# Kernel optimization log

Hardware: AMD Instinct MI355X
Metric: run time of the kernel (lower is better)

Reference implementation:

```python
import jax, jax.numpy as jnp
import numpy as np

N_NODES = 50000
N_EDGES = 800000
IN_C, HID, OUT_C = 128, 128, 16
N_GRAPHS = 128


def setup_inputs() -> dict:
    key = jax.random.key(0)
    ks = jax.random.split(key, 8)
    x = jax.random.normal(ks[0], (N_NODES, IN_C), dtype=jnp.float32)
    edge_index = jax.random.randint(ks[1], (2, N_EDGES), 0, N_NODES, dtype=jnp.int64)
    batch = jnp.sort(jax.random.randint(ks[2], (N_NODES,), 0, N_GRAPHS, dtype=jnp.int64))
    s1 = 1.0 / np.sqrt(IN_C)
    s2 = 1.0 / np.sqrt(HID)
    W1 = jax.random.normal(ks[3], (IN_C, HID), dtype=jnp.float32) * s1
    b1 = jnp.zeros((HID,), dtype=jnp.float32)
    W2 = jax.random.normal(ks[4], (HID, HID), dtype=jnp.float32) * s2
    b2 = jnp.zeros((HID,), dtype=jnp.float32)
    Wfc = jax.random.normal(ks[5], (HID, OUT_C), dtype=jnp.float32) * s2
    bfc = jnp.zeros((OUT_C,), dtype=jnp.float32)
    return {"x": x, "edge_index": edge_index, "batch": batch,
            "W1": W1, "b1": b1, "W2": W2, "b2": b2, "Wfc": Wfc, "bfc": bfc}


def _gcn_conv(x, W, b, src, dst, deg_inv_sqrt, n_nodes):
    # linear transform first (PyG order), then normalized sparse aggregation
    h = x @ W  # [N, H]
    norm = deg_inv_sqrt[src] * deg_inv_sqrt[dst]  # [E+N] (self-loops appended)
    msgs = h[src] * norm[:, None]  # [E+N, H] dominant gather
    agg = jax.ops.segment_sum(msgs, dst, num_segments=n_nodes)
    return agg + b


def reference(x, edge_index, batch, W1, b1, W2, b2, Wfc, bfc):
    n = x.shape[0]
    loops = jnp.arange(n, dtype=edge_index.dtype)
    src = jnp.concatenate([edge_index[0], loops])
    dst = jnp.concatenate([edge_index[1], loops])
    # symmetric normalization with self-loops: deg computed on dst
    deg = jax.ops.segment_sum(jnp.ones_like(src, dtype=x.dtype), dst, num_segments=n)
    deg_inv_sqrt = jnp.where(deg > 0, jax.lax.rsqrt(jnp.maximum(deg, 1.0)), 0.0)

    h = jax.nn.relu(_gcn_conv(x, W1, b1, src, dst, deg_inv_sqrt, n))
    h = jax.nn.relu(_gcn_conv(h, W2, b2, src, dst, deg_inv_sqrt, n))

    # global mean pool over graph ids
    sums = jax.ops.segment_sum(h, batch, num_segments=N_GRAPHS)
    counts = jax.ops.segment_sum(jnp.ones((n,), dtype=h.dtype), batch, num_segments=N_GRAPHS)
    pooled = sums / jnp.maximum(counts, 1.0)[:, None]  # [G, H]

    logits = pooled @ Wfc + bfc  # [G, OUT_C]
    return jax.nn.log_softmax(logits, axis=1)
```

## Files before the change

kernel.cpp:

```cpp
#include <hip/hip_runtime.h>

#define N_NODES  50000
#define N_EDGES  800000
#define HID      128
#define OUT_C    16
#define N_GRAPHS 128
#define MAXDEG   64
#define NSLICE   6250
#define EPB      8192

typedef __attribute__((ext_vector_type(8))) short bf16x8;
typedef __attribute__((ext_vector_type(4))) float f32x4;
typedef __attribute__((ext_vector_type(8))) unsigned short us8;
typedef __attribute__((ext_vector_type(4))) unsigned short us4;

__device__ __forceinline__ unsigned short f2bf(float f) {
  unsigned u = __float_as_uint(f);
  u += 0x7fffu + ((u >> 16) & 1u);
  return (unsigned short)(u >> 16);
}

__global__ __launch_bounds__(256) void fill_deg_kernel(
    const int* __restrict__ src, const int* __restrict__ dst,
    int* __restrict__ deg, unsigned short* __restrict__ ell) {
  const int slice = blockIdx.x & 7;
  const int e0 = (blockIdx.x >> 3) * EPB;
  const int e1 = min(e0 + EPB, N_EDGES);
  const unsigned lo = slice * NSLICE;
  for (int e = e0 + threadIdx.x; e < e1; e += 256) {
    int d = dst[e];
    if ((unsigned)(d - lo) < (unsigned)NSLICE) {
      int p = atomicAdd(&deg[d], 1);
      if (p < MAXDEG) ell[(d << 6) + p] = (unsigned short)src[e];
    }
  }
}

__global__ void prep_kernel(const float* __restrict__ W1, const float* __restrict__ W2,
                            unsigned short* __restrict__ wt1, unsigned short* __restrict__ wt2,
                            const int* __restrict__ deg, float* __restrict__ dis,
                            const int* __restrict__ batch, int* __restrict__ start) {
  int b = blockIdx.x;
  if (b < 128) {
    int idx = b * 256 + threadIdx.x;
    int sel = idx >> 14;
    int r = idx & 16383;
    int k = r >> 7, n = r & 127;
    const float* W = sel ? W2 : W1;
    unsigned short* wt = sel ? wt2 : wt1;
    wt[n * HID + k] = f2bf(W[k * HID + n]);
  } else if (b < 324) {
    int i = (b - 128) * 256 + threadIdx.x;
    if (i < N_NODES) dis[i] = rsqrtf((float)deg[i] + 1.0f);
  } else {
    int t = threadIdx.x;
    if (t <= N_GRAPHS) {
      int lo = 0, hi = N_NODES;
      while (lo < hi) {
        int mid = (lo + hi) >> 1;
        if (batch[mid] < t) lo = mid + 1; else hi = mid;
      }
      start[t] = lo;
    }
  }
}

#define PAD 136
__global__ __launch_bounds__(256) void gemm_mfma_kernel(
    const float* __restrict__ H, const unsigned short* __restrict__ Wt,
    unsigned short* __restrict__ T, int n_nodes) {
  __shared__ unsigned short sA[64 * PAD];
  __shared__ unsigned short sW[128 * PAD];
  const int tid = threadIdx.x;
  const int lane = tid & 63;
  const int w = tid >> 6;
  const int l15 = lane & 15;
  const int quad = lane >> 4;
  const int base = blockIdx.x * 64;

#pragma unroll
  for (int i = 0; i < 8; ++i) {
    int idx = tid + i * 256;
    int row = idx >> 4;
    int col = (idx & 15) * 8;
    *(us8*)(sW + row * PAD + col) = *(const us8*)(Wt + row * HID + col);
  }
#pragma unroll
  for (int i = 0; i < 8; ++i) {
    int idx = tid + i * 256;
    int nrow = idx >> 5;
    int c4 = (idx & 31) * 4;
    float4 v = make_float4(0.f, 0.f, 0.f, 0.f);
    int node = base + nrow;
    if (node < n_nodes) v = *(const float4*)(H + (size_t)node * HID + c4);
    us4 b;
    b.x = f2bf(v.x); b.y = f2bf(v.y); b.z = f2bf(v.z); b.w = f2bf(v.w);
    *(us4*)(sA + nrow * PAD + c4) = b;
  }
  __syncthreads();

  f32x4 acc[4][2];
#pragma unroll
  for (int nt = 0; nt < 4; ++nt)
#pragma unroll
    for (int c = 0; c < 2; ++c) acc[nt][c] = (f32x4)(0.f);

  const int ct0 = w * 2;
#pragma unroll
  for (int ks = 0; ks < 4; ++ks) {
    int koff = ks * 32 + quad * 8;
    bf16x8 a[4], bfr[2];
#pragma unroll
    for (int nt = 0; nt < 4; ++nt)
      a[nt] = *(const bf16x8*)(sA + (nt * 16 + l15) * PAD + koff);
#pragma unroll
    for (int c = 0; c < 2; ++c)
      bfr[c] = *(const bf16x8*)(sW + ((ct0 + c) * 16 + l15) * PAD + koff);
#pragma unroll
    for (int nt = 0; nt < 4; ++nt)
#pragma unroll
      for (int c = 0; c < 2; ++c)
        acc[nt][c] = __builtin_amdgcn_mfma_f32_16x16x32_bf16(a[nt], bfr[c], acc[nt][c], 0, 0, 0);
  }
  __syncthreads();

#pragma unroll
  for (int nt = 0; nt < 4; ++nt)
#pragma unroll
    for (int c = 0; c < 2; ++c)
#pragma unroll
      for (int r = 0; r < 4; ++r)
        sA[(nt * 16 + quad * 4 + r) * PAD + (ct0 + c) * 16 + l15] = f2bf(acc[nt][c][r]);
  __syncthreads();
#pragma unroll
  for (int i = 0; i < 4; ++i) {
    int idx = tid + i * 256;
    int nrow = idx >> 4;
    int col = (idx & 15) * 8;
    int node = base + nrow;
    if (node < n_nodes)
      *(us8*)(T + (size_t)node * HID + col) = *(const us8*)(sA + nrow * PAD + col);
  }
}

__global__ __launch_bounds__(256) void aggregate_kernel(
    const unsigned int* __restrict__ Tb, const unsigned short* __restrict__ ell,
    const int* __restrict__ deg, const float* __restrict__ dis,
    const float* __restrict__ bias, float* __restrict__ Hout) {
  int node = (blockIdx.x * blockDim.x + threadIdx.x) >> 6;
  int lane = threadIdx.x & 63;
  if (node >= N_NODES) return;
  float dd = dis[node];
  float2 b = ((const float2*)bias)[lane];
  unsigned sv = Tb[(size_t)node * 64 + lane];
  float wself = dd * dd;
  float ax = __int_as_float(sv << 16) * wself;
  float ay = __int_as_float(sv & 0xffff0000u) * wself;
  int m = min(deg[node], MAXDEG);
  int s0 = node << 6;
  int sidx = 0; float wv = 0.f;
  if (lane < m) {
    sidx = (int)ell[s0 + lane];
    wv = dis[sidx] * dd;
  }
  int j = 0;
  for (; j + 8 <= m; j += 8) {
#pragma unroll
    for (int q = 0; q < 8; ++q) {
      int s = __builtin_amdgcn_readlane(sidx, j + q);
      float w = __int_as_float(__builtin_amdgcn_readlane(__float_as_int(wv), j + q));
      unsigned t = Tb[(size_t)s * 64 + lane];
      ax += w * __int_as_float(t << 16);
      ay += w * __int_as_float(t & 0xffff0000u);
    }
  }
  for (; j < m; ++j) {
    int s = __builtin_amdgcn_readlane(sidx, j);
    float w = __int_as_float(__builtin_amdgcn_readlane(__float_as_int(wv), j));
    unsigned t = Tb[(size_t)s * 64 + lane];
    ax += w * __int_as_float(t << 16);
    ay += w * __int_as_float(t & 0xffff0000u);
  }
  float2 o;
  o.x = fmaxf(ax + b.x, 0.f);
  o.y = fmaxf(ay + b.y, 0.f);
  ((float2*)Hout)[(size_t)node * 64 + lane] = o;
}

__global__ __launch_bounds__(256) void pool_kernel(
    const float* __restrict__ H, const int* __restrict__ start,
    float* __restrict__ pooled) {
  __shared__ float2 red[4][64];
  int g = blockIdx.x;
  int n0 = start[g], n1 = start[g + 1];
  int lane = threadIdx.x & 63, w = threadIdx.x >> 6;
  const float2* __restrict__ H2 = (const float2*)H;
  float ax = 0.f, ay = 0.f;
  for (int n = n0 + w; n < n1; n += 4) {
    float2 h = H2[(size_t)n * 64 + lane];
    ax += h.x; ay += h.y;
  }
  red[w][lane] = make_float2(ax, ay);
  __syncthreads();
  if (threadIdx.x < 64) {
    float2 a = red[0][lane], b1 = red[1][lane], c = red[2][lane], d = red[3][lane];
    float inv = 1.0f / fmaxf((float)(n1 - n0), 1.0f);
    float2 o;
    o.x = (a.x + b1.x + c.x + d.x) * inv;
    o.y = (a.y + b1.y + c.y + d.y) * inv;
    ((float2*)pooled)[g * 64 + lane] = o;
  }
}

__global__ __launch_bounds__(64) void head_kernel(
    const float* __restrict__ pooled, const float* __restrict__ Wfc,
    const float* __restrict__ bfc, float* __restrict__ out) {
  int g = blockIdx.x;
  int lane = threadIdx.x;
  int o = lane & 15;
  float part = 0.f;
  for (int k = (lane >> 4); k < HID; k += 4)
    part += pooled[g * HID + k] * Wfc[k * OUT_C + o];
  part += __shfl_xor(part, 16);
  part += __shfl_xor(part, 32);
  float logit = part + bfc[o];
  float m = logit;
#pragma unroll
  for (int d = 8; d >= 1; d >>= 1) m = fmaxf(m, __shfl_xor(m, d, 16));
  float e = __expf(logit - m);
  float s = e;
#pragma unroll
  for (int d = 8; d >= 1; d >>= 1) s += __shfl_xor(s, d, 16);
  float r = logit - m - __logf(s);
  if (lane < 16) out[g * OUT_C + o] = r;
}

extern "C" void kernel_launch(void* const* d_in, const int* in_sizes, int n_in,
                              void* d_out, int out_size, void* d_ws, size_t ws_size,
                              hipStream_t stream) {
  const float* x    = (const float*)d_in[0];
  const int*   ei   = (const int*)d_in[1];
  const int*   batch= (const int*)d_in[2];
  const float* W1   = (const float*)d_in[3];
  const float* b1   = (const float*)d_in[4];
  const float* W2   = (const float*)d_in[5];
  const float* b2   = (const float*)d_in[6];
  const float* Wfc  = (const float*)d_in[7];
  const float* bfc  = (const float*)d_in[8];
  float* out = (float*)d_out;
  const int* src = ei;
  const int* dst = ei + N_EDGES;

  char* p = (char*)d_ws;
  auto alloc = [&](size_t bytes) { char* r = p; p += (bytes + 255) & ~255ull; return r; };
  int*   degI   = (int*)alloc((size_t)N_NODES * 4);
  float* dis    = (float*)alloc((size_t)N_NODES * 4);
  int*   start  = (int*)alloc((N_GRAPHS + 1) * 4);
  float* pooled = (float*)alloc((size_t)N_GRAPHS * HID * 4);
  unsigned short* ell = (unsigned short*)alloc((size_t)N_NODES * MAXDEG * 2);
  unsigned short* wt1 = (unsigned short*)alloc((size_t)HID * HID * 2);
  unsigned short* wt2 = (unsigned short*)alloc((size_t)HID * HID * 2);
  unsigned short* T   = (unsigned short*)alloc((size_t)N_NODES * HID * 2);
  float* H      = (float*)alloc((size_t)N_NODES * HID * 4);

  hipMemsetAsync(degI, 0, (size_t)N_NODES * 4, stream);

  int fill_blocks = ((N_EDGES + EPB - 1) / EPB) * 8;

  fill_deg_kernel<<<fill_blocks, 256, 0, stream>>>(src, dst, degI, ell);
  prep_kernel<<<325, 256, 0, stream>>>(W1, W2, wt1, wt2, degI, dis, batch, start);

  int gemm_blocks = (N_NODES + 63) / 64;
  int agg_blocks  = (N_NODES * 64 + 255) / 256;

  gemm_mfma_kernel<<<gemm_blocks, 256, 0, stream>>>(x, wt1, T, N_NODES);
  aggregate_kernel<<<agg_blocks, 256, 0, stream>>>((const unsigned int*)T, ell, degI, dis, b1, H);
  gemm_mfma_kernel<<<gemm_blocks, 256, 0, stream>>>(H, wt2, T, N_NODES);
  aggregate_kernel<<<agg_blocks, 256, 0, stream>>>((const unsigned int*)T, ell, degI, dis, b2, H);

  pool_kernel<<<N_GRAPHS, 256, 0, stream>>>(H, start, pooled);
  head_kernel<<<N_GRAPHS, 64, 0, stream>>>(pooled, Wfc, bfc, out);
}
```

Before: 262.5 us.

## Build ELL adjacency per node window in shared memory after compacting dst

Replaces the global-atomic ELL fill with a two-step scheme. First the destination indices are compacted to 16-bit. Then each block owns a 200-node window, scans all edges, counts degrees and places neighbours with shared-memory atomics, and writes its ELL rows and degrees out with coalesced stores. This removes global atomics, scattered ELL writes and the degree memset. In exchange, each of 250 blocks re-reads the whole 1.6 MB dst16 array, and src is still read per match.

```diff
diff --git a/kernel.cpp b/kernel.cpp
--- a/kernel.cpp
+++ b/kernel.cpp
@@ -6,8 +6,7 @@
 #define OUT_C    16
 #define N_GRAPHS 128
 #define MAXDEG   64
-#define NSLICE   6250
-#define EPB      8192
+#define WIN      200
 
 typedef __attribute__((ext_vector_type(8))) short bf16x8;
 typedef __attribute__((ext_vector_type(4))) float f32x4;
@@ -20,20 +19,48 @@
   return (unsigned short)(u >> 16);
 }
 
-__global__ __launch_bounds__(256) void fill_deg_kernel(
-    const int* __restrict__ src, const int* __restrict__ dst,
+__global__ __launch_bounds__(256) void compact_kernel(
+    const int* __restrict__ dst, unsigned short* __restrict__ dst16) {
+  int i = blockIdx.x * 256 + threadIdx.x;
+  if (i < N_EDGES / 4) {
+    int4 d = ((const int4*)dst)[i];
+    us4 o;
+    o.x = (unsigned short)d.x; o.y = (unsigned short)d.y;
+    o.z = (unsigned short)d.z; o.w = (unsigned short)d.w;
+    *(us4*)(dst16 + i * 4) = o;
+  }
+}
+
+__global__ __launch_bounds__(256) void fill_win_kernel(
+    const int* __restrict__ src, const unsigned short* __restrict__ dst16,
     int* __restrict__ deg, unsigned short* __restrict__ ell) {
-  const int slice = blockIdx.x & 7;
-  const int e0 = (blockIdx.x >> 3) * EPB;
-  const int e1 = min(e0 + EPB, N_EDGES);
-  const unsigned lo = slice * NSLICE;
-  for (int e = e0 + threadIdx.x; e < e1; e += 256) {
-    int d = dst[e];
-    if ((unsigned)(d - lo) < (unsigned)NSLICE) {
-      int p = atomicAdd(&deg[d], 1);
-      if (p < MAXDEG) ell[(d << 6) + p] = (unsigned short)src[e];
+  __shared__ unsigned short sell[WIN * MAXDEG];
+  __shared__ int sdeg[WIN];
+  const int n0 = blockIdx.x * WIN;
+  for (int i = threadIdx.x; i < WIN; i += 256) sdeg[i] = 0;
+  __syncthreads();
+  const us8* __restrict__ d8 = (const us8*)dst16;
+  for (int q = threadIdx.x; q < N_EDGES / 8; q += 256) {
+    us8 d = d8[q];
+    int e = q * 8;
+#pragma unroll
+    for (int j = 0; j < 8; ++j) {
+      unsigned r = (unsigned)((int)d[j] - n0);
+      if (r < (unsigned)WIN) {
+        int p = atomicAdd(&sdeg[r], 1);
+        if (p < MAXDEG) sell[(r << 6) + p] = (unsigned short)src[e + j];
+      }
     }
   }
+  __syncthreads();
+  for (int i = threadIdx.x; i < WIN; i += 256) {
+    int n = n0 + i;
+    if (n < N_NODES) deg[n] = sdeg[i];
+  }
+  us8* __restrict__ eo = (us8*)(ell + (size_t)n0 * MAXDEG);
+  const us8* __restrict__ ei8 = (const us8*)sell;
+  for (int i = threadIdx.x; i < WIN * MAXDEG / 8; i += 256)
+    eo[i] = ei8[i];
 }
 
 __global__ void prep_kernel(const float* __restrict__ W1, const float* __restrict__ W2,
@@ -257,17 +284,15 @@
   float* dis    = (float*)alloc((size_t)N_NODES * 4);
   int*   start  = (int*)alloc((N_GRAPHS + 1) * 4);
   float* pooled = (float*)alloc((size_t)N_GRAPHS * HID * 4);
+  unsigned short* dst16 = (unsigned short*)alloc((size_t)N_EDGES * 2);
   unsigned short* ell = (unsigned short*)alloc((size_t)N_NODES * MAXDEG * 2);
   unsigned short* wt1 = (unsigned short*)alloc((size_t)HID * HID * 2);
   unsigned short* wt2 = (unsigned short*)alloc((size_t)HID * HID * 2);
   unsigned short* T   = (unsigned short*)alloc((size_t)N_NODES * HID * 2);
   float* H      = (float*)alloc((size_t)N_NODES * HID * 4);
 
-  hipMemsetAsync(degI, 0, (size_t)N_NODES * 4, stream);
-
-  int fill_blocks = ((N_EDGES + EPB - 1) / EPB) * 8;
-
-  fill_deg_kernel<<<fill_blocks, 256, 0, stream>>>(src, dst, degI, ell);
+  compact_kernel<<<(N_EDGES / 4 + 255) / 256, 256, 0, stream>>>(dst, dst16);
+  fill_win_kernel<<<N_NODES / WIN, 256, 0, stream>>>(src, dst16, degI, ell);
   prep_kernel<<<325, 256, 0, stream>>>(W1, W2, wt1, wt2, degI, dis, batch, start);
 
   int gemm_blocks = (N_NODES + 63) / 64;
```

After: 492.2 us. 1.87x slower.

## Fuse fill, graph-start search and first GEMM into one launch; merge pool and head

Applied to the files above, without the earlier changes.

Merges the degree/ELL fill, graph-start search and the first layer GEMM into one kernel, since they are independent and can run as different block ranges. Each GEMM block now reads and transposes fp32 weights to bf16 itself instead of using a separate prep pass. The aggregation recomputes rsqrt of degree inline instead of reading a precomputed array, and pooling is fused with the FC/log-softmax head. This cuts the launch count from eight to five at the cost of redundant weight conversion per block and extra rsqrt work per edge.

```diff
diff --git a/kernel.cpp b/kernel.cpp
--- a/kernel.cpp
+++ b/kernel.cpp
@@ -8,6 +8,9 @@
 #define MAXDEG   64
 #define NSLICE   6250
 #define EPB      8192
+#define FILLB    784
+#define GEMMB    782
+#define PAD      136
 
 typedef __attribute__((ext_vector_type(8))) short bf16x8;
 typedef __attribute__((ext_vector_type(4))) float f32x4;
@@ -20,11 +23,11 @@
   return (unsigned short)(u >> 16);
 }
 
-__global__ __launch_bounds__(256) void fill_deg_kernel(
-    const int* __restrict__ src, const int* __restrict__ dst,
+__device__ __forceinline__ void fill_body(
+    int b, const int* __restrict__ src, const int* __restrict__ dst,
     int* __restrict__ deg, unsigned short* __restrict__ ell) {
-  const int slice = blockIdx.x & 7;
-  const int e0 = (blockIdx.x >> 3) * EPB;
+  const int slice = b & 7;
+  const int e0 = (b >> 3) * EPB;
   const int e1 = min(e0 + EPB, N_EDGES);
   const unsigned lo = slice * NSLICE;
   for (int e = e0 + threadIdx.x; e < e1; e += 256) {
@@ -36,54 +39,28 @@
   }
 }
 
-__global__ void prep_kernel(const float* __restrict__ W1, const float* __restrict__ W2,
-                            unsigned short* __restrict__ wt1, unsigned short* __restrict__ wt2,
-                            const int* __restrict__ deg, float* __restrict__ dis,
-                            const int* __restrict__ batch, int* __restrict__ start) {
-  int b = blockIdx.x;
-  if (b < 128) {
-    int idx = b * 256 + threadIdx.x;
-    int sel = idx >> 14;
-    int r = idx & 16383;
-    int k = r >> 7, n = r & 127;
-    const float* W = sel ? W2 : W1;
-    unsigned short* wt = sel ? wt2 : wt1;
-    wt[n * HID + k] = f2bf(W[k * HID + n]);
-  } else if (b < 324) {
-    int i = (b - 128) * 256 + threadIdx.x;
-    if (i < N_NODES) dis[i] = rsqrtf((float)deg[i] + 1.0f);
-  } else {
-    int t = threadIdx.x;
-    if (t <= N_GRAPHS) {
-      int lo = 0, hi = N_NODES;
-      while (lo < hi) {
-        int mid = (lo + hi) >> 1;
-        if (batch[mid] < t) lo = mid + 1; else hi = mid;
-      }
-      start[t] = lo;
-    }
-  }
-}
-
-#define PAD 136
-__global__ __launch_bounds__(256) void gemm_mfma_kernel(
-    const float* __restrict__ H, const unsigned short* __restrict__ Wt,
-    unsigned short* __restrict__ T, int n_nodes) {
-  __shared__ unsigned short sA[64 * PAD];
-  __shared__ unsigned short sW[128 * PAD];
+__device__ __forceinline__ void gemm_body(
+    int blk, const float* __restrict__ H, const float* __restrict__ W,
+    unsigned short* __restrict__ T, int n_nodes, unsigned short* smem) {
+  unsigned short* sA = smem;
+  unsigned short* sW = smem + 64 * PAD;
   const int tid = threadIdx.x;
   const int lane = tid & 63;
   const int w = tid >> 6;
   const int l15 = lane & 15;
   const int quad = lane >> 4;
-  const int base = blockIdx.x * 64;
-
-#pragma unroll
-  for (int i = 0; i < 8; ++i) {
+  const int base = blk * 64;
+
+#pragma unroll
+  for (int i = 0; i < 16; ++i) {
     int idx = tid + i * 256;
-    int row = idx >> 4;
-    int col = (idx & 15) * 8;
-    *(us8*)(sW + row * PAD + col) = *(const us8*)(Wt + row * HID + col);
+    int k = idx >> 5;
+    int n0 = (idx & 31) << 2;
+    float4 v = *(const float4*)(W + (size_t)k * HID + n0);
+    sW[(n0 + 0) * PAD + k] = f2bf(v.x);
+    sW[(n0 + 1) * PAD + k] = f2bf(v.y);
+    sW[(n0 + 2) * PAD + k] = f2bf(v.z);
+    sW[(n0 + 3) * PAD + k] = f2bf(v.w);
   }
 #pragma unroll
   for (int i = 0; i < 8; ++i) {
@@ -143,25 +120,58 @@
   }
 }
 
+__global__ __launch_bounds__(256) void mega1_kernel(
+    const int* __restrict__ src, const int* __restrict__ dst,
+    int* __restrict__ deg, unsigned short* __restrict__ ell,
+    const int* __restrict__ batch, int* __restrict__ start,
+    const float* __restrict__ x, const float* __restrict__ W1,
+    unsigned short* __restrict__ T) {
+  __shared__ unsigned short smem[192 * PAD];
+  int b = blockIdx.x;
+  if (b < FILLB) {
+    fill_body(b, src, dst, deg, ell);
+  } else if (b == FILLB) {
+    int t = threadIdx.x;
+    if (t <= N_GRAPHS) {
+      int lo = 0, hi = N_NODES;
+      while (lo < hi) {
+        int mid = (lo + hi) >> 1;
+        if (batch[mid] < t) lo = mid + 1; else hi = mid;
+      }
+      start[t] = lo;
+    }
+  } else {
+    gemm_body(b - FILLB - 1, x, W1, T, N_NODES, smem);
+  }
+}
+
+__global__ __launch_bounds__(256) void gemm_kernel(
+    const float* __restrict__ H, const float* __restrict__ W,
+    unsigned short* __restrict__ T) {
+  __shared__ unsigned short smem[192 * PAD];
+  gemm_body(blockIdx.x, H, W, T, N_NODES, smem);
+}
+
 __global__ __launch_bounds__(256) void aggregate_kernel(
     const unsigned int* __restrict__ Tb, const unsigned short* __restrict__ ell,
-    const int* __restrict__ deg, const float* __restrict__ dis,
-    const float* __restrict__ bias, float* __restrict__ Hout) {
+    const int* __restrict__ deg, const float* __restrict__ bias,
+    float* __restrict__ Hout) {
   int node = (blockIdx.x * blockDim.x + threadIdx.x) >> 6;
   int lane = threadIdx.x & 63;
   if (node >= N_NODES) return;
-  float dd = dis[node];
+  int dn = deg[node];
+  float dd = rsqrtf((float)dn + 1.0f);
   float2 b = ((const float2*)bias)[lane];
   unsigned sv = Tb[(size_t)node * 64 + lane];
   float wself = dd * dd;
   float ax = __int_as_float(sv << 16) * wself;
   float ay = __int_as_float(sv & 0xffff0000u) * wself;
-  int m = min(deg[node], MAXDEG);
+  int m = min(dn, MAXDEG);
   int s0 = node << 6;
   int sidx = 0; float wv = 0.f;
   if (lane < m) {
     sidx = (int)ell[s0 + lane];
-    wv = dis[sidx] * dd;
+    wv = rsqrtf((float)deg[sidx] + 1.0f) * dd;
   }
   int j = 0;
   for (; j + 8 <= m; j += 8) {
@@ -187,10 +197,12 @@
   ((float2*)Hout)[(size_t)node * 64 + lane] = o;
 }
 
-__global__ __launch_bounds__(256) void pool_kernel(
+__global__ __launch_bounds__(256) void pool_head_kernel(
     const float* __restrict__ H, const int* __restrict__ start,
-    float* __restrict__ pooled) {
+    const float* __restrict__ Wfc, const float* __restrict__ bfc,
+    float* __restrict__ out) {
   __shared__ float2 red[4][64];
+  __shared__ float spool[HID];
   int g = blockIdx.x;
   int n0 = start[g], n1 = start[g + 1];
   int lane = threadIdx.x & 63, w = threadIdx.x >> 6;
@@ -205,34 +217,28 @@
   if (threadIdx.x < 64) {
     float2 a = red[0][lane], b1 = red[1][lane], c = red[2][lane], d = red[3][lane];
     float inv = 1.0f / fmaxf((float)(n1 - n0), 1.0f);
-    float2 o;
-    o.x = (a.x + b1.x + c.x + d.x) * inv;
-    o.y = (a.y + b1.y + c.y + d.y) * inv;
-    ((float2*)pooled)[g * 64 + lane] = o;
-  }
-}
-
-__global__ __launch_bounds__(64) void head_kernel(
-    const float* __restrict__ pooled, const float* __restrict__ Wfc,
-    const float* __restrict__ bfc, float* __restrict__ out) {
-  int g = blockIdx.x;
-  int lane = threadIdx.x;
-  int o = lane & 15;
-  float part = 0.f;
-  for (int k = (lane >> 4); k < HID; k += 4)
-    part += pooled[g * HID + k] * Wfc[k * OUT_C + o];
-  part += __shfl_xor(part, 16);
-  part += __shfl_xor(part, 32);
-  float logit = part + bfc[o];
-  float m = logit;
-#pragma unroll
-  for (int d = 8; d >= 1; d >>= 1) m = fmaxf(m, __shfl_xor(m, d, 16));
-  float e = __expf(logit - m);
-  float s = e;
-#pragma unroll
-  for (int d = 8; d >= 1; d >>= 1) s += __shfl_xor(s, d, 16);
-  float r = logit - m - __logf(s);
-  if (lane < 16) out[g * OUT_C + o] = r;
+    spool[lane * 2]     = (a.x + b1.x + c.x + d.x) * inv;
+    spool[lane * 2 + 1] = (a.y + b1.y + c.y + d.y) * inv;
+  }
+  __syncthreads();
+  if (threadIdx.x < 64) {
+    int o = lane & 15;
+    float part = 0.f;
+    for (int k = (lane >> 4); k < HID; k += 4)
+      part += spool[k] * Wfc[k * OUT_C + o];
+    part += __shfl_xor(part, 16);
+    part += __shfl_xor(part, 32);
+    float logit = part + bfc[o];
+    float m = logit;
+#pragma unroll
+    for (int d = 8; d >= 1; d >>= 1) m = fmaxf(m, __shfl_xor(m, d, 16));
+    float e = __expf(logit - m);
+    float s = e;
+#pragma unroll
+    for (int d = 8; d >= 1; d >>= 1) s += __shfl_xor(s, d, 16);
+    float r = logit - m - __logf(s);
+    if (lane < 16) out[g * OUT_C + o] = r;
+  }
 }
 
 extern "C" void kernel_launch(void* const* d_in, const int* in_sizes, int n_in,
@@ -254,30 +260,19 @@
   char* p = (char*)d_ws;
   auto alloc = [&](size_t bytes) { char* r = p; p += (bytes + 255) & ~255ull; return r; };
   int*   degI   = (int*)alloc((size_t)N_NODES * 4);
-  float* dis    = (float*)alloc((size_t)N_NODES * 4);
   int*   start  = (int*)alloc((N_GRAPHS + 1) * 4);
-  float* pooled = (float*)alloc((size_t)N_GRAPHS * HID * 4);
   unsigned short* ell = (unsigned short*)alloc((size_t)N_NODES * MAXDEG * 2);
-  unsigned short* wt1 = (unsigned short*)alloc((size_t)HID * HID * 2);
-  unsigned short* wt2 = (unsigned short*)alloc((size_t)HID * HID * 2);
   unsigned short* T   = (unsigned short*)alloc((size_t)N_NODES * HID * 2);
   float* H      = (float*)alloc((size_t)N_NODES * HID * 4);
 
   hipMemsetAsync(degI, 0, (size_t)N_NODES * 4, stream);
 
-  int fill_blocks = ((N_EDGES + EPB - 1) / EPB) * 8;
-
-  fill_deg_kernel<<<fill_blocks, 256, 0, stream>>>(src, dst, degI, ell);
-  prep_kernel<<<325, 256, 0, stream>>>(W1, W2, wt1, wt2, degI, dis, batch, start);
-
-  int gemm_blocks = (N_NODES + 63) / 64;
-  int agg_blocks  = (N_NODES * 64 + 255) / 256;
-
-  gemm_mfma_kernel<<<gemm_blocks, 256, 0, stream>>>(x, wt1, T, N_NODES);
-  aggregate_kernel<<<agg_blocks, 256, 0, stream>>>((const unsigned int*)T, ell, degI, dis, b1, H);
-  gemm_mfma_kernel<<<gemm_blocks, 256, 0, stream>>>(H, wt2, T, N_NODES);
-  aggregate_kernel<<<agg_blocks, 256, 0, stream>>>((const unsigned int*)T, ell, degI, dis, b2, H);
-
-  pool_kernel<<<N_GRAPHS, 256, 0, stream>>>(H, start, pooled);
-  head_kernel<<<N_GRAPHS, 64, 0, stream>>>(pooled, Wfc, bfc, out);
-}
+  int agg_blocks = (N_NODES * 64 + 255) / 256;
+
+  mega1_kernel<<<FILLB + 1 + GEMMB, 256, 0, stream>>>(src, dst, degI, ell,
+                                                      batch, start, x, W1, T);
+  aggregate_kernel<<<agg_blocks, 256, 0, stream>>>((const unsigned int*)T, ell, degI, b1, H);
+  gemm_kernel<<<GEMMB, 256, 0, stream>>>(H, W2, T);
+  aggregate_kernel<<<agg_blocks, 256, 0, stream>>>((const unsigned int*)T, ell, degI, b2, H);
+  pool_head_kernel<<<N_GRAPHS, 256, 0, stream>>>(H, start, Wfc, bfc, out);
+}
```

Measured after the change: 272.1 us. 1.04x slower.
